# Performance work log

Hardware: AMD Instinct MI355X
Metric: run time of the kernel (lower is better)

The kernel has to match this reference:

```python
import jax, jax.numpy as jnp
import numpy as np

N = 100000      # nodes
E = 1600000     # edges (avg degree 16)
F_IN = 128
F_HID = 128
LN_EPS = 1e-5


def setup_inputs() -> dict:
    key = jax.random.key(0)
    ks = jax.random.split(key, 4)
    x = jax.random.normal(ks[0], (N, F_IN), dtype=jnp.float32)
    edge_index = jax.random.randint(ks[1], (2, E), 0, N, dtype=jnp.int32)
    W1 = jax.random.normal(ks[2], (F_IN, F_HID), dtype=jnp.float32) * 0.05
    W2 = jax.random.normal(ks[3], (F_HID, F_HID), dtype=jnp.float32) * 0.05
    return {
        "x": x,
        "edge_index": edge_index,
        "W1": W1, "b1": jnp.zeros((F_HID,), jnp.float32),
        "W2": W2, "b2": jnp.zeros((F_HID,), jnp.float32),
        "g1": jnp.ones((F_HID,), jnp.float32), "be1": jnp.zeros((F_HID,), jnp.float32),
        "g2": jnp.ones((F_HID,), jnp.float32), "be2": jnp.zeros((F_HID,), jnp.float32),
    }


def layer_norm(x, gamma, beta):
    mu = jnp.mean(x, axis=-1, keepdims=True)
    var = jnp.mean(jnp.square(x - mu), axis=-1, keepdims=True)
    return (x - mu) * jax.lax.rsqrt(var + LN_EPS) * gamma + beta


def gcn_conv(x, src, dst, W, b):
    """PyG GCNConv: linear transform, add self-loops, symmetric-normalized scatter-add."""
    n = x.shape[0]
    loop = jnp.arange(n, dtype=src.dtype)
    s = jnp.concatenate([src, loop])   # [E+N] sources (incl. self-loops)
    d = jnp.concatenate([dst, loop])   # [E+N] destinations
    deg = jax.ops.segment_sum(jnp.ones(s.shape[0], x.dtype), d, num_segments=n)
    dinv = jnp.where(deg > 0, jax.lax.rsqrt(deg), 0.0)
    norm = dinv[s] * dinv[d]           # [E+N] edge normalization
    h = x @ W                          # [N, F_hid] transform BEFORE propagate (PyG order)
    msg = h[s] * norm[:, None]         # [E+N, F_hid] gathered, normalized messages
    out = jax.ops.segment_sum(msg, d, num_segments=n)
    return out + b


def reference(x, edge_index, W1, b1, W2, b2, g1, be1, g2, be2):
    # GCN_body, layer=2, layer_norm_first=False, use_ln=True, eval mode (dropout=identity)
    src, dst = edge_index[0], edge_index[1]
    h = layer_norm(jax.nn.relu(gcn_conv(x, src, dst, W1, b1)), g1, be1)
    h = layer_norm(jax.nn.relu(gcn_conv(h, src, dst, W2, b2)), g2, be2)
    return h
```

## Files before the change

### kernel.cpp

```cpp
#include <hip/hip_runtime.h>

#define FDIM 128
#define LN_EPS 1e-5f

typedef short short8 __attribute__((ext_vector_type(8)));
typedef float f32x4 __attribute__((ext_vector_type(4)));

__device__ __forceinline__ ushort f2bf(float f) {
    uint u = __float_as_uint(f);
    u += 0x7fff + ((u >> 16) & 1);
    return (ushort)(u >> 16);
}
__device__ __forceinline__ float bflo(uint u) { return __uint_as_float(u << 16); }
__device__ __forceinline__ float bfhi(uint u) { return __uint_as_float(u & 0xffff0000u); }

__global__ void k_count(const int* __restrict__ dst, int* __restrict__ cnt,
                        int* __restrict__ pos, int E) {
    int e = blockIdx.x * 256 + threadIdx.x;
    if (e < E) pos[e] = atomicAdd(&cnt[dst[e]], 1);
}

__global__ __launch_bounds__(1024) void k_scan_block(const int* __restrict__ cnt,
                                                     int* __restrict__ rowptr,
                                                     int* __restrict__ partial, int N) {
    __shared__ int s[1024];
    int t = threadIdx.x;
    int i = blockIdx.x * 1024 + t;
    int v = (i < N) ? ((cnt[i] + 7) & ~7) : 0;
    s[t] = v;
    __syncthreads();
    for (int off = 1; off < 1024; off <<= 1) {
        int u = (t >= off) ? s[t - off] : 0;
        __syncthreads();
        s[t] += u;
        __syncthreads();
    }
    if (i < N) rowptr[i] = s[t] - v;
    if (t == 1023) partial[blockIdx.x] = s[1023];
}

__global__ __launch_bounds__(1024) void k_scan_partial(int* __restrict__ partial, int NB) {
    __shared__ int s[1024];
    int t = threadIdx.x;
    int v = (t < NB) ? partial[t] : 0;
    s[t] = v;
    __syncthreads();
    for (int off = 1; off < 1024; off <<= 1) {
        int u = (t >= off) ? s[t - off] : 0;
        __syncthreads();
        s[t] += u;
        __syncthreads();
    }
    if (t < NB) partial[t] = s[t] - v;
}

__global__ void k_finalize(int* __restrict__ rowptr, const int* __restrict__ partial,
                           const int* __restrict__ cnt, float* __restrict__ dinv,
                           int* __restrict__ col, int N, int E) {
    int i = blockIdx.x * 256 + threadIdx.x;
    if (i < N) {
        int rp = rowptr[i] + partial[i >> 10];
        rowptr[i] = rp;
        int deg = cnt[i];
        int deg8 = (deg + 7) & ~7;
        dinv[i] = rsqrtf((float)deg + 1.0f);
        for (int k = deg; k < deg8; ++k) col[rp + k] = N;
        if (i == N - 1) rowptr[N] = rp + deg8;
    }
}

__global__ void k_fill(const int* __restrict__ src, const int* __restrict__ dst,
                       const int* __restrict__ rowptr, const int* __restrict__ pos,
                       int* __restrict__ col, int E) {
    int e = blockIdx.x * 256 + threadIdx.x;
    if (e < E) col[rowptr[dst[e]] + pos[e]] = src[e];
}

__global__ void k_wt2(const float* __restrict__ W1, const float* __restrict__ W2,
                      ushort* __restrict__ WT1, ushort* __restrict__ WT2) {
    int b = blockIdx.x, k = threadIdx.x;
    if (b < 128) WT1[b * 128 + k] = f2bf(W1[k * 128 + b]);
    else         WT2[(b - 128) * 128 + k] = f2bf(W2[k * 128 + (b - 128)]);
}

template <bool F32IN>
__global__ __launch_bounds__(256) void k_gemm(const void* __restrict__ Xin,
                                              const ushort* __restrict__ WT,
                                              const float* __restrict__ dinv,
                                              ushort* __restrict__ H, int N) {
    __shared__ ushort sX[64 * 128];
    __shared__ ushort sW[128 * 128];
    char* sXb = (char*)sX;
    char* sWb = (char*)sW;

    int t = threadIdx.x;
    int w = t >> 6, lane = t & 63;
    int cl = lane & 15, kq = lane >> 4;
    int base = blockIdx.x * 64;

    const short8* Wg = (const short8*)WT;
#pragma unroll
    for (int k = 0; k < 8; ++k) {
        int idx = t + k * 256;
        int c = idx >> 4, ch = idx & 15;
        *(short8*)(sWb + c * 256 + ((ch * 16) ^ ((c & 7) << 4))) = Wg[idx];
    }

    if constexpr (F32IN) {
        const float4* X4 = (const float4*)Xin;
        size_t lim = (size_t)N * 32 - 1;
#pragma unroll
        for (int k = 0; k < 8; ++k) {
            int idx = t + k * 256;
            size_t gi = (size_t)base * 32 + idx;
            float4 v = X4[gi < lim ? gi : lim];
            ushort4 o;
            o.x = f2bf(v.x); o.y = f2bf(v.y); o.z = f2bf(v.z); o.w = f2bf(v.w);
            int row = idx >> 5, b8 = (idx & 31) * 8;
            *(ushort4*)(sXb + row * 256 + (b8 ^ ((row & 7) << 4))) = o;
        }
    } else {
        const short8* X8 = (const short8*)Xin;
        size_t lim = (size_t)N * 16 - 1;
#pragma unroll
        for (int k = 0; k < 4; ++k) {
            int idx = t + k * 256;
            size_t gi = (size_t)base * 16 + idx;
            short8 v = X8[gi < lim ? gi : lim];
            int row = idx >> 4, b16 = (idx & 15) * 16;
            *(short8*)(sXb + row * 256 + (b16 ^ ((row & 7) << 4))) = v;
        }
    }
    __syncthreads();

    int rl = w * 16 + cl;
    short8 b0, b1, b2, b3;
#pragma unroll
    for (int kt = 0; kt < 4; ++kt) {
        short8 v = *(const short8*)(sXb + rl * 256 + ((kt * 64 + kq * 16) ^ ((rl & 7) << 4)));
        if (kt == 0) b0 = v; else if (kt == 1) b1 = v; else if (kt == 2) b2 = v; else b3 = v;
    }

    int r = base + rl;
    bool ok = r < N;
    float di = dinv[min(r, N - 1)];
#pragma unroll
    for (int nt = 0; nt < 8; ++nt) {
        int c = nt * 16 + cl;
        int sw = (c & 7) << 4;
        f32x4 acc = {0.f, 0.f, 0.f, 0.f};
        acc = __builtin_amdgcn_mfma_f32_16x16x32_bf16(
            *(const short8*)(sWb + c * 256 + ((0 * 64 + kq * 16) ^ sw)), b0, acc, 0, 0, 0);
        acc = __builtin_amdgcn_mfma_f32_16x16x32_bf16(
            *(const short8*)(sWb + c * 256 + ((1 * 64 + kq * 16) ^ sw)), b1, acc, 0, 0, 0);
        acc = __builtin_amdgcn_mfma_f32_16x16x32_bf16(
            *(const short8*)(sWb + c * 256 + ((2 * 64 + kq * 16) ^ sw)), b2, acc, 0, 0, 0);
        acc = __builtin_amdgcn_mfma_f32_16x16x32_bf16(
            *(const short8*)(sWb + c * 256 + ((3 * 64 + kq * 16) ^ sw)), b3, acc, 0, 0, 0);
        if (ok) {
            ushort4 o;
            o.x = f2bf(acc[0] * di); o.y = f2bf(acc[1] * di);
            o.z = f2bf(acc[2] * di); o.w = f2bf(acc[3] * di);
            *(ushort4*)(H + (size_t)r * 128 + nt * 16 + kq * 4) = o;
        }
    }
}

__global__ __launch_bounds__(256) void k_agg(const uint2* __restrict__ H2,
                                             const int* __restrict__ rowptr,
                                             const int* __restrict__ col,
                                             const float* __restrict__ dinv,
                                             const float* __restrict__ bias,
                                             const float* __restrict__ gamma,
                                             const float* __restrict__ beta,
                                             float* __restrict__ outf,
                                             uint2* __restrict__ outb,
                                             int N) {
    int wave = threadIdx.x >> 6;
    int lane = threadIdx.x & 63;
    int half = lane >> 5;
    int l = lane & 31;
    int node = blockIdx.x * 8 + wave * 2 + half;
    bool valid = node < N;
    int nodec = valid ? node : N - 1;

    float di = dinv[nodec];
    uint2 hs = H2[(uint)nodec * 32u + (uint)l];
    float ax = bflo(hs.x), ay = bfhi(hs.x);
    float az = bflo(hs.y), aw = bfhi(hs.y);

    int beg = rowptr[nodec];
    int deg8 = rowptr[nodec + 1] - beg;
    const int* cp = col + beg;

    for (int i = 0; i < deg8; i += 8) {
        int s0 = cp[i + 0], s1 = cp[i + 1], s2 = cp[i + 2], s3 = cp[i + 3];
        int s4 = cp[i + 4], s5 = cp[i + 5], s6 = cp[i + 6], s7 = cp[i + 7];
        uint2 u0 = H2[(uint)s0 * 32u + (uint)l];
        uint2 u1 = H2[(uint)s1 * 32u + (uint)l];
        uint2 u2 = H2[(uint)s2 * 32u + (uint)l];
        uint2 u3 = H2[(uint)s3 * 32u + (uint)l];
        uint2 u4 = H2[(uint)s4 * 32u + (uint)l];
        uint2 u5 = H2[(uint)s5 * 32u + (uint)l];
        uint2 u6 = H2[(uint)s6 * 32u + (uint)l];
        uint2 u7 = H2[(uint)s7 * 32u + (uint)l];
        ax += bflo(u0.x); ay += bfhi(u0.x); az += bflo(u0.y); aw += bfhi(u0.y);
        ax += bflo(u1.x); ay += bfhi(u1.x); az += bflo(u1.y); aw += bfhi(u1.y);
        ax += bflo(u2.x); ay += bfhi(u2.x); az += bflo(u2.y); aw += bfhi(u2.y);
        ax += bflo(u3.x); ay += bfhi(u3.x); az += bflo(u3.y); aw += bfhi(u3.y);
        ax += bflo(u4.x); ay += bfhi(u4.x); az += bflo(u4.y); aw += bfhi(u4.y);
        ax += bflo(u5.x); ay += bfhi(u5.x); az += bflo(u5.y); aw += bfhi(u5.y);
        ax += bflo(u6.x); ay += bfhi(u6.x); az += bflo(u6.y); aw += bfhi(u6.y);
        ax += bflo(u7.x); ay += bfhi(u7.x); az += bflo(u7.y); aw += bfhi(u7.y);
    }

    float4 bb = ((const float4*)bias)[l];
    float a0 = fmaxf(fmaf(ax, di, bb.x), 0.f);
    float a1 = fmaxf(fmaf(ay, di, bb.y), 0.f);
    float a2 = fmaxf(fmaf(az, di, bb.z), 0.f);
    float a3 = fmaxf(fmaf(aw, di, bb.w), 0.f);

    float s1 = a0 + a1 + a2 + a3;
    float s2 = a0 * a0 + a1 * a1 + a2 * a2 + a3 * a3;
#pragma unroll
    for (int off = 16; off >= 1; off >>= 1) {
        s1 += __shfl_xor(s1, off);
        s2 += __shfl_xor(s2, off);
    }
    float mu = s1 * (1.f / 128.f);
    float var = s2 * (1.f / 128.f) - mu * mu;
    float rs = rsqrtf(var + LN_EPS);

    float4 g = ((const float4*)gamma)[l];
    float4 be = ((const float4*)beta)[l];
    float o0 = (a0 - mu) * rs * g.x + be.x;
    float o1 = (a1 - mu) * rs * g.y + be.y;
    float o2 = (a2 - mu) * rs * g.z + be.z;
    float o3 = (a3 - mu) * rs * g.w + be.w;

    if (!valid) return;
    if (outf) {
        ((float4*)outf)[(size_t)node * 32 + l] = make_float4(o0, o1, o2, o3);
    } else {
        uint2 o;
        o.x = (uint)f2bf(o0) | ((uint)f2bf(o1) << 16);
        o.y = (uint)f2bf(o2) | ((uint)f2bf(o3) << 16);
        outb[(size_t)node * 32 + l] = o;
    }
}

extern "C" void kernel_launch(void* const* d_in, const int* in_sizes, int n_in,
                              void* d_out, int out_size, void* d_ws, size_t ws_size,
                              hipStream_t stream) {
    const float* x  = (const float*)d_in[0];
    const int*   ei = (const int*)d_in[1];
    const float* W1 = (const float*)d_in[2];
    const float* b1 = (const float*)d_in[3];
    const float* W2 = (const float*)d_in[4];
    const float* b2 = (const float*)d_in[5];
    const float* g1 = (const float*)d_in[6];
    const float* be1 = (const float*)d_in[7];
    const float* g2 = (const float*)d_in[8];
    const float* be2 = (const float*)d_in[9];

    int N = in_sizes[0] / FDIM;
    int E = in_sizes[1] / 2;
    const int* srcp = ei;
    const int* dstp = ei + E;
    float* out = (float*)d_out;

    char* w = (char*)d_ws;
    size_t off = 0;
    auto take = [&](size_t bytes) {
        void* p = w + off;
        off = (off + bytes + 255) & ~(size_t)255;
        return p;
    };
    ushort* hb   = (ushort*)take((size_t)(N + 1) * FDIM * sizeof(ushort));
    ushort* WT1  = (ushort*)take(128 * 128 * sizeof(ushort));
    ushort* WT2  = (ushort*)take(128 * 128 * sizeof(ushort));
    int* cnt     = (int*)take((size_t)N * sizeof(int));
    int* rowptr  = (int*)take((size_t)(N + 1) * sizeof(int));
    int* pos     = (int*)take((size_t)E * sizeof(int));
    int* colb    = (int*)take((size_t)(E + 7 * (size_t)N + 8) * sizeof(int));
    float* dinv  = (float*)take((size_t)N * sizeof(float));
    int* partial = (int*)take(1024 * sizeof(int));
    (void)ws_size;

    int NB = (N + 1023) >> 10;

    hipMemsetAsync(cnt, 0, (size_t)N * sizeof(int), stream);
    hipMemsetAsync(hb + (size_t)N * FDIM, 0, FDIM * sizeof(ushort), stream);

    k_count<<<(E + 255) / 256, 256, 0, stream>>>(dstp, cnt, pos, E);
    k_scan_block<<<NB, 1024, 0, stream>>>(cnt, rowptr, partial, N);
    k_scan_partial<<<1, 1024, 0, stream>>>(partial, NB);
    k_finalize<<<(N + 255) / 256, 256, 0, stream>>>(rowptr, partial, cnt, dinv, colb, N, E);
    k_fill<<<(E + 255) / 256, 256, 0, stream>>>(srcp, dstp, rowptr, pos, colb, E);

    k_wt2<<<256, 128, 0, stream>>>(W1, W2, WT1, WT2);

    k_gemm<true><<<(N + 63) / 64, 256, 0, stream>>>(x, WT1, dinv, hb, N);
    k_agg<<<(N + 7) / 8, 256, 0, stream>>>((const uint2*)hb, rowptr, colb, dinv,
                                           b1, g1, be1, nullptr, (uint2*)d_out, N);
    k_gemm<false><<<(N + 63) / 64, 256, 0, stream>>>(d_out, WT2, dinv, hb, N);
    k_agg<<<(N + 7) / 8, 256, 0, stream>>>((const uint2*)hb, rowptr, colb, dinv,
                                           b2, g2, be2, out, nullptr, N);
}
```

Measured before the change: 269.6 us.

## Fuse CSR fill with first GEMM, shrink pos to ushort, widen agg gathers

The CSR column-fill work and the first-layer GEMM now run as block ranges of one merged launch, so the two independent stages overlap and one kernel launch is removed. The per-edge position array is stored as ushort instead of int, halving its write and read traffic; this is only correct while every node's in-degree stays below 65536. The aggregation kernel now uses 16 lanes per node with 16-byte gathers instead of 32 lanes with 8-byte gathers, which means fewer, wider memory requests per neighbour row and a shorter reduction. The merged kernel reserves GEMM-sized shared memory even for the fill blocks, which may limit how many of those blocks fit per compute unit.

```diff
diff --git a/kernel.cpp b/kernel.cpp
--- a/kernel.cpp
+++ b/kernel.cpp
@@ -15,9 +15,9 @@
 __device__ __forceinline__ float bfhi(uint u) { return __uint_as_float(u & 0xffff0000u); }
 
 __global__ void k_count(const int* __restrict__ dst, int* __restrict__ cnt,
-                        int* __restrict__ pos, int E) {
+                        ushort* __restrict__ pos, int E) {
     int e = blockIdx.x * 256 + threadIdx.x;
-    if (e < E) pos[e] = atomicAdd(&cnt[dst[e]], 1);
+    if (e < E) pos[e] = (ushort)atomicAdd(&cnt[dst[e]], 1);
 }
 
 __global__ __launch_bounds__(1024) void k_scan_block(const int* __restrict__ cnt,
@@ -69,13 +69,6 @@
     }
 }
 
-__global__ void k_fill(const int* __restrict__ src, const int* __restrict__ dst,
-                       const int* __restrict__ rowptr, const int* __restrict__ pos,
-                       int* __restrict__ col, int E) {
-    int e = blockIdx.x * 256 + threadIdx.x;
-    if (e < E) col[rowptr[dst[e]] + pos[e]] = src[e];
-}
-
 __global__ void k_wt2(const float* __restrict__ W1, const float* __restrict__ W2,
                       ushort* __restrict__ WT1, ushort* __restrict__ WT2) {
     int b = blockIdx.x, k = threadIdx.x;
@@ -84,19 +77,15 @@
 }
 
 template <bool F32IN>
-__global__ __launch_bounds__(256) void k_gemm(const void* __restrict__ Xin,
-                                              const ushort* __restrict__ WT,
-                                              const float* __restrict__ dinv,
-                                              ushort* __restrict__ H, int N) {
-    __shared__ ushort sX[64 * 128];
-    __shared__ ushort sW[128 * 128];
-    char* sXb = (char*)sX;
-    char* sWb = (char*)sW;
-
+__device__ __forceinline__ void gemm_body(char* sXb, char* sWb,
+                                          const void* __restrict__ Xin,
+                                          const ushort* __restrict__ WT,
+                                          const float* __restrict__ dinv,
+                                          ushort* __restrict__ H, int N, int bid) {
     int t = threadIdx.x;
     int w = t >> 6, lane = t & 63;
     int cl = lane & 15, kq = lane >> 4;
-    int base = blockIdx.x * 64;
+    int base = bid * 64;
 
     const short8* Wg = (const short8*)WT;
 #pragma unroll
@@ -166,7 +155,36 @@
     }
 }
 
-__global__ __launch_bounds__(256) void k_agg(const uint2* __restrict__ H2,
+template <bool F32IN>
+__global__ __launch_bounds__(256) void k_gemm(const void* __restrict__ Xin,
+                                              const ushort* __restrict__ WT,
+                                              const float* __restrict__ dinv,
+                                              ushort* __restrict__ H, int N) {
+    __shared__ ushort sX[64 * 128];
+    __shared__ ushort sW[128 * 128];
+    gemm_body<F32IN>((char*)sX, (char*)sW, Xin, WT, dinv, H, N, blockIdx.x);
+}
+
+__global__ __launch_bounds__(256) void k_mega(const void* __restrict__ Xin,
+                                              const ushort* __restrict__ WT,
+                                              const float* __restrict__ dinv,
+                                              ushort* __restrict__ H, int N, int ngemm,
+                                              const int* __restrict__ src,
+                                              const int* __restrict__ dst,
+                                              const int* __restrict__ rowptr,
+                                              const ushort* __restrict__ pos,
+                                              int* __restrict__ col, int E) {
+    __shared__ ushort sX[64 * 128];
+    __shared__ ushort sW[128 * 128];
+    if (blockIdx.x < (uint)ngemm) {
+        gemm_body<true>((char*)sX, (char*)sW, Xin, WT, dinv, H, N, blockIdx.x);
+    } else {
+        int e = (blockIdx.x - ngemm) * 256 + threadIdx.x;
+        if (e < E) col[rowptr[dst[e]] + (int)pos[e]] = src[e];
+    }
+}
+
+__global__ __launch_bounds__(256) void k_agg(const uint4* __restrict__ H4,
                                              const int* __restrict__ rowptr,
                                              const int* __restrict__ col,
                                              const float* __restrict__ dinv,
@@ -174,20 +192,20 @@
                                              const float* __restrict__ gamma,
                                              const float* __restrict__ beta,
                                              float* __restrict__ outf,
-                                             uint2* __restrict__ outb,
+                                             uint4* __restrict__ outb,
                                              int N) {
     int wave = threadIdx.x >> 6;
     int lane = threadIdx.x & 63;
-    int half = lane >> 5;
-    int l = lane & 31;
-    int node = blockIdx.x * 8 + wave * 2 + half;
+    int q = lane >> 4;
+    int l = lane & 15;
+    int node = blockIdx.x * 16 + wave * 4 + q;
     bool valid = node < N;
     int nodec = valid ? node : N - 1;
 
     float di = dinv[nodec];
-    uint2 hs = H2[(uint)nodec * 32u + (uint)l];
-    float ax = bflo(hs.x), ay = bfhi(hs.x);
-    float az = bflo(hs.y), aw = bfhi(hs.y);
+    uint4 hs = H4[(uint)nodec * 16u + (uint)l];
+    float a0 = bflo(hs.x), a1 = bfhi(hs.x), a2 = bflo(hs.y), a3 = bfhi(hs.y);
+    float a4 = bflo(hs.z), a5 = bfhi(hs.z), a6 = bflo(hs.w), a7 = bfhi(hs.w);
 
     int beg = rowptr[nodec];
     int deg8 = rowptr[nodec + 1] - beg;
@@ -196,34 +214,48 @@
     for (int i = 0; i < deg8; i += 8) {
         int s0 = cp[i + 0], s1 = cp[i + 1], s2 = cp[i + 2], s3 = cp[i + 3];
         int s4 = cp[i + 4], s5 = cp[i + 5], s6 = cp[i + 6], s7 = cp[i + 7];
-        uint2 u0 = H2[(uint)s0 * 32u + (uint)l];
-        uint2 u1 = H2[(uint)s1 * 32u + (uint)l];
-        uint2 u2 = H2[(uint)s2 * 32u + (uint)l];
-        uint2 u3 = H2[(uint)s3 * 32u + (uint)l];
-        uint2 u4 = H2[(uint)s4 * 32u + (uint)l];
-        uint2 u5 = H2[(uint)s5 * 32u + (uint)l];
-        uint2 u6 = H2[(uint)s6 * 32u + (uint)l];
-        uint2 u7 = H2[(uint)s7 * 32u + (uint)l];
-        ax += bflo(u0.x); ay += bfhi(u0.x); az += bflo(u0.y); aw += bfhi(u0.y);
-        ax += bflo(u1.x); ay += bfhi(u1.x); az += bflo(u1.y); aw += bfhi(u1.y);
-        ax += bflo(u2.x); ay += bfhi(u2.x); az += bflo(u2.y); aw += bfhi(u2.y);
-        ax += bflo(u3.x); ay += bfhi(u3.x); az += bflo(u3.y); aw += bfhi(u3.y);
-        ax += bflo(u4.x); ay += bfhi(u4.x); az += bflo(u4.y); aw += bfhi(u4.y);
-        ax += bflo(u5.x); ay += bfhi(u5.x); az += bflo(u5.y); aw += bfhi(u5.y);
-        ax += bflo(u6.x); ay += bfhi(u6.x); az += bflo(u6.y); aw += bfhi(u6.y);
-        ax += bflo(u7.x); ay += bfhi(u7.x); az += bflo(u7.y); aw += bfhi(u7.y);
-    }
-
-    float4 bb = ((const float4*)bias)[l];
-    float a0 = fmaxf(fmaf(ax, di, bb.x), 0.f);
-    float a1 = fmaxf(fmaf(ay, di, bb.y), 0.f);
-    float a2 = fmaxf(fmaf(az, di, bb.z), 0.f);
-    float a3 = fmaxf(fmaf(aw, di, bb.w), 0.f);
-
-    float s1 = a0 + a1 + a2 + a3;
-    float s2 = a0 * a0 + a1 * a1 + a2 * a2 + a3 * a3;
-#pragma unroll
-    for (int off = 16; off >= 1; off >>= 1) {
+        uint4 u0 = H4[(uint)s0 * 16u + (uint)l];
+        uint4 u1 = H4[(uint)s1 * 16u + (uint)l];
+        uint4 u2 = H4[(uint)s2 * 16u + (uint)l];
+        uint4 u3 = H4[(uint)s3 * 16u + (uint)l];
+        uint4 u4 = H4[(uint)s4 * 16u + (uint)l];
+        uint4 u5 = H4[(uint)s5 * 16u + (uint)l];
+        uint4 u6 = H4[(uint)s6 * 16u + (uint)l];
+        uint4 u7 = H4[(uint)s7 * 16u + (uint)l];
+        a0 += bflo(u0.x); a1 += bfhi(u0.x); a2 += bflo(u0.y); a3 += bfhi(u0.y);
+        a4 += bflo(u0.z); a5 += bfhi(u0.z); a6 += bflo(u0.w); a7 += bfhi(u0.w);
+        a0 += bflo(u1.x); a1 += bfhi(u1.x); a2 += bflo(u1.y); a3 += bfhi(u1.y);
+        a4 += bflo(u1.z); a5 += bfhi(u1.z); a6 += bflo(u1.w); a7 += bfhi(u1.w);
+        a0 += bflo(u2.x); a1 += bfhi(u2.x); a2 += bflo(u2.y); a3 += bfhi(u2.y);
+        a4 += bflo(u2.z); a5 += bfhi(u2.z); a6 += bflo(u2.w); a7 += bfhi(u2.w);
+        a0 += bflo(u3.x); a1 += bfhi(u3.x); a2 += bflo(u3.y); a3 += bfhi(u3.y);
+        a4 += bflo(u3.z); a5 += bfhi(u3.z); a6 += bflo(u3.w); a7 += bfhi(u3.w);
+        a0 += bflo(u4.x); a1 += bfhi(u4.x); a2 += bflo(u4.y); a3 += bfhi(u4.y);
+        a4 += bflo(u4.z); a5 += bfhi(u4.z); a6 += bflo(u4.w); a7 += bfhi(u4.w);
+        a0 += bflo(u5.x); a1 += bfhi(u5.x); a2 += bflo(u5.y); a3 += bfhi(u5.y);
+        a4 += bflo(u5.z); a5 += bfhi(u5.z); a6 += bflo(u5.w); a7 += bfhi(u5.w);
+        a0 += bflo(u6.x); a1 += bfhi(u6.x); a2 += bflo(u6.y); a3 += bfhi(u6.y);
+        a4 += bflo(u6.z); a5 += bfhi(u6.z); a6 += bflo(u6.w); a7 += bfhi(u6.w);
+        a0 += bflo(u7.x); a1 += bfhi(u7.x); a2 += bflo(u7.y); a3 += bfhi(u7.y);
+        a4 += bflo(u7.z); a5 += bfhi(u7.z); a6 += bflo(u7.w); a7 += bfhi(u7.w);
+    }
+
+    float4 bb0 = ((const float4*)bias)[2 * l];
+    float4 bb1 = ((const float4*)bias)[2 * l + 1];
+    a0 = fmaxf(fmaf(a0, di, bb0.x), 0.f);
+    a1 = fmaxf(fmaf(a1, di, bb0.y), 0.f);
+    a2 = fmaxf(fmaf(a2, di, bb0.z), 0.f);
+    a3 = fmaxf(fmaf(a3, di, bb0.w), 0.f);
+    a4 = fmaxf(fmaf(a4, di, bb1.x), 0.f);
+    a5 = fmaxf(fmaf(a5, di, bb1.y), 0.f);
+    a6 = fmaxf(fmaf(a6, di, bb1.z), 0.f);
+    a7 = fmaxf(fmaf(a7, di, bb1.w), 0.f);
+
+    float s1 = ((a0 + a1) + (a2 + a3)) + ((a4 + a5) + (a6 + a7));
+    float s2 = ((a0 * a0 + a1 * a1) + (a2 * a2 + a3 * a3)) +
+               ((a4 * a4 + a5 * a5) + (a6 * a6 + a7 * a7));
+#pragma unroll
+    for (int off = 8; off >= 1; off >>= 1) {
         s1 += __shfl_xor(s1, off);
         s2 += __shfl_xor(s2, off);
     }
@@ -231,21 +263,30 @@
     float var = s2 * (1.f / 128.f) - mu * mu;
     float rs = rsqrtf(var + LN_EPS);
 
-    float4 g = ((const float4*)gamma)[l];
-    float4 be = ((const float4*)beta)[l];
-    float o0 = (a0 - mu) * rs * g.x + be.x;
-    float o1 = (a1 - mu) * rs * g.y + be.y;
-    float o2 = (a2 - mu) * rs * g.z + be.z;
-    float o3 = (a3 - mu) * rs * g.w + be.w;
+    float4 g0 = ((const float4*)gamma)[2 * l];
+    float4 g1 = ((const float4*)gamma)[2 * l + 1];
+    float4 e0 = ((const float4*)beta)[2 * l];
+    float4 e1 = ((const float4*)beta)[2 * l + 1];
+    float o0 = (a0 - mu) * rs * g0.x + e0.x;
+    float o1 = (a1 - mu) * rs * g0.y + e0.y;
+    float o2 = (a2 - mu) * rs * g0.z + e0.z;
+    float o3 = (a3 - mu) * rs * g0.w + e0.w;
+    float o4 = (a4 - mu) * rs * g1.x + e1.x;
+    float o5 = (a5 - mu) * rs * g1.y + e1.y;
+    float o6 = (a6 - mu) * rs * g1.z + e1.z;
+    float o7 = (a7 - mu) * rs * g1.w + e1.w;
 
     if (!valid) return;
     if (outf) {
-        ((float4*)outf)[(size_t)node * 32 + l] = make_float4(o0, o1, o2, o3);
+        ((float4*)outf)[(size_t)node * 32 + 2 * l]     = make_float4(o0, o1, o2, o3);
+        ((float4*)outf)[(size_t)node * 32 + 2 * l + 1] = make_float4(o4, o5, o6, o7);
     } else {
-        uint2 o;
+        uint4 o;
         o.x = (uint)f2bf(o0) | ((uint)f2bf(o1) << 16);
         o.y = (uint)f2bf(o2) | ((uint)f2bf(o3) << 16);
-        outb[(size_t)node * 32 + l] = o;
+        o.z = (uint)f2bf(o4) | ((uint)f2bf(o5) << 16);
+        o.w = (uint)f2bf(o6) | ((uint)f2bf(o7) << 16);
+        outb[(size_t)node * 16 + l] = o;
     }
 }
 
@@ -281,29 +322,32 @@
     ushort* WT2  = (ushort*)take(128 * 128 * sizeof(ushort));
     int* cnt     = (int*)take((size_t)N * sizeof(int));
     int* rowptr  = (int*)take((size_t)(N + 1) * sizeof(int));
-    int* pos     = (int*)take((size_t)E * sizeof(int));
+    ushort* pos  = (ushort*)take((size_t)E * sizeof(ushort));
     int* colb    = (int*)take((size_t)(E + 7 * (size_t)N + 8) * sizeof(int));
     float* dinv  = (float*)take((size_t)N * sizeof(float));
     int* partial = (int*)take(1024 * sizeof(int));
     (void)ws_size;
 
     int NB = (N + 1023) >> 10;
+    int ngemm = (N + 63) / 64;
+    int nfill = (E + 255) / 256;
 
     hipMemsetAsync(cnt, 0, (size_t)N * sizeof(int), stream);
     hipMemsetAsync(hb + (size_t)N * FDIM, 0, FDIM * sizeof(ushort), stream);
+
+    k_wt2<<<256, 128, 0, stream>>>(W1, W2, WT1, WT2);
 
     k_count<<<(E + 255) / 256, 256, 0, stream>>>(dstp, cnt, pos, E);
     k_scan_block<<<NB, 1024, 0, stream>>>(cnt, rowptr, partial, N);
     k_scan_partial<<<1, 1024, 0, stream>>>(partial, NB);
     k_finalize<<<(N + 255) / 256, 256, 0, stream>>>(rowptr, partial, cnt, dinv, colb, N, E);
-    k_fill<<<(E + 255) / 256, 256, 0, stream>>>(srcp, dstp, rowptr, pos, colb, E);
-
-    k_wt2<<<256, 128, 0, stream>>>(W1, W2, WT1, WT2);
-
-    k_gemm<true><<<(N + 63) / 64, 256, 0, stream>>>(x, WT1, dinv, hb, N);
-    k_agg<<<(N + 7) / 8, 256, 0, stream>>>((const uint2*)hb, rowptr, colb, dinv,
-                                           b1, g1, be1, nullptr, (uint2*)d_out, N);
-    k_gemm<false><<<(N + 63) / 64, 256, 0, stream>>>(d_out, WT2, dinv, hb, N);
-    k_agg<<<(N + 7) / 8, 256, 0, stream>>>((const uint2*)hb, rowptr, colb, dinv,
-                                           b2, g2, be2, out, nullptr, N);
-}
+
+    k_mega<<<ngemm + nfill, 256, 0, stream>>>(x, WT1, dinv, hb, N, ngemm,
+                                              srcp, dstp, rowptr, pos, colb, E);
+
+    k_agg<<<(N + 15) / 16, 256, 0, stream>>>((const uint4*)hb, rowptr, colb, dinv,
+                                             b1, g1, be1, nullptr, (uint4*)d_out, N);
+    k_gemm<false><<<ngemm, 256, 0, stream>>>(d_out, WT2, dinv, hb, N);
+    k_agg<<<(N + 15) / 16, 256, 0, stream>>>((const uint4*)hb, rowptr, colb, dinv,
+                                             b2, g2, be2, out, nullptr, N);
+}
```

Result: faster. 260.6 us (-3.4%).
